# Optimization experiments

Measured on AMD Instinct MI355X. Metric: run time of the kernel, lower is better.

Reference implementation:

```python
import jax, jax.numpy as jnp
import numpy as np

N_NODES = 10000
N_EDGES = 320000
D_IN = 256
D_HID = 256
N_CLASSES = 40


def _init_linear(key, fan_in, fan_out):
    kw, kb = jax.random.split(key)
    bound = 1.0 / np.sqrt(fan_in)
    W = jax.random.uniform(kw, (fan_in, fan_out), jnp.float32, -bound, bound)
    b = jax.random.uniform(kb, (fan_out,), jnp.float32, -bound, bound)
    return W, b


def setup_inputs() -> dict:
    key = jax.random.key(0)
    k0, k1, k2, k3, k4 = jax.random.split(key, 5)
    node_features = jax.random.normal(k0, (N_NODES, D_IN), jnp.float32)
    edge_index = jax.random.randint(k1, (2, N_EDGES), 0, N_NODES, jnp.int64)
    W1, b1 = _init_linear(k2, D_IN, D_HID)
    W2, b2 = _init_linear(k3, D_HID, D_HID)
    W3, b3 = _init_linear(k4, D_HID, N_CLASSES)
    return {"node_features": node_features, "edge_index": edge_index,
            "W1": W1, "b1": b1, "W2": W2, "b2": b2, "W3": W3, "b3": b3}


def _mp_layer(x, src, dst, W, b):
    # message: linear transform of source-node features (transform-then-gather
    # is mathematically identical to gather-then-transform and cheaper when E>N)
    msg = (x @ W + b)[src]                      # [E, d_out]
    # scatter sum-aggregate messages at destination nodes
    out = jax.ops.segment_sum(msg, dst, num_segments=N_NODES)  # [N, d_out]
    return out


def reference(node_features, edge_index, W1, b1, W2, b2, W3, b3):
    src, dst = edge_index[0], edge_index[1]
    x = jax.nn.relu(_mp_layer(node_features, src, dst, W1, b1))
    x = jax.nn.relu(_mp_layer(x, src, dst, W2, b2))
    x = jax.nn.relu(_mp_layer(x, src, dst, W3, b3))
    return x
```

## Files before the change

### kernel.cpp

```cpp
#include <hip/hip_runtime.h>


#define N_NODES   10000
#define N_EDGES   320000
#define D_HID     256
#define N_CLASSES 40
#define CAP       96

typedef __attribute__((ext_vector_type(8))) short short8;
typedef __attribute__((ext_vector_type(4))) float f32x4;

__device__ __forceinline__ ushort f2bf(float f) {
    unsigned u = __float_as_uint(f);
    u = (u + 0x7fffu + ((u >> 16) & 1u)) >> 16;
    return (ushort)u;
}
__device__ __forceinline__ float bf2f(ushort u) {
    return __uint_as_float(((unsigned)u) << 16);
}


__global__ __launch_bounds__(256)
void prep_kernel(const float* __restrict__ X,
                 const float* __restrict__ W1, const float* __restrict__ W2,
                 const float* __restrict__ W3,
                 ushort* __restrict__ Xb, ushort* __restrict__ bufY,
                 ushort* __restrict__ bufH,
                 ushort* __restrict__ W1b, ushort* __restrict__ W2b,
                 ushort* __restrict__ W3b, int* __restrict__ cursor,
                 int* __restrict__ esrc) {
    const int tid  = blockIdx.x * 256 + threadIdx.x;
    const int nthr = gridDim.x * 256;
    for (int i = tid; i < N_NODES; i += nthr) cursor[i] = 0;
    for (int i = tid; i < N_NODES * CAP; i += nthr) esrc[i] = N_NODES;
    ushort4 z; z.x = 0; z.y = 0; z.z = 0; z.w = 0;
    if (tid < 64) {
        ((ushort4*)Xb)[640000 + tid]   = z;
        ((ushort4*)bufY)[640000 + tid] = z;
    }
    if (tid < 10) ((ushort4*)bufH)[100000 + tid] = z;
    for (int i = tid; i < N_NODES * D_HID / 4; i += nthr) {
        float4 v = ((const float4*)X)[i];
        ushort4 o;
        o.x = f2bf(v.x); o.y = f2bf(v.y); o.z = f2bf(v.z); o.w = f2bf(v.w);
        ((ushort4*)Xb)[i] = o;
    }
    for (int i = tid; i < 141312; i += nthr) {
        if (i < 65536) {
            int n = i >> 8, k = i & 255;
            W1b[i] = f2bf(W1[k * 256 + n]);
        } else if (i < 131072) {
            int t2 = i - 65536;
            int n = t2 >> 8, k = t2 & 255;
            W2b[t2] = f2bf(W2[k * 256 + n]);
        } else {
            int t2 = i - 131072;
            int n = t2 >> 8, k = t2 & 255;
            W3b[t2] = f2bf(W3[k * N_CLASSES + n]);
        }
    }
}


__global__ __launch_bounds__(256)
void place_kernel(const int* __restrict__ edges, int* __restrict__ cursor,
                  int* __restrict__ esrc) {
    int e = blockIdx.x * 256 + threadIdx.x;
    if (e < N_EDGES) {
        int d = edges[N_EDGES + e];
        int pos = atomicAdd(&cursor[d], 1);
        if (pos < CAP) esrc[d * CAP + pos] = edges[e];
    }
}


__global__ __launch_bounds__(256)
void gather_kernel(const ushort* __restrict__ Xin, const int* __restrict__ deg,
                   const int* __restrict__ esrc, ushort* __restrict__ Ag) {
    __shared__ int eidx[4 * CAP];
    __shared__ int degL[4];

    const int tid  = threadIdx.x;
    const int w    = tid >> 6, lane = tid & 63;
    const int lo   = lane & 31, hi = lane >> 5;
    const int base = blockIdx.x * 4;

    for (int i = tid; i < 4 * CAP; i += 256) eidx[i] = esrc[base * CAP + i];
    if (tid < 4) {
        int c = deg[base + tid];
        degL[tid] = (c > CAP) ? CAP : c;
    }
    __syncthreads();

    const int node = base + w;
    const int nb   = (degL[w] + 15) >> 4;
    const uint4* hp4 = (const uint4*)Xin;

    float a[8] = {};
    for (int b = 0; b < nb; ++b) {
        uint4 v[8];
#pragma unroll
        for (int u = 0; u < 8; ++u) {
            int e = eidx[w * CAP + b * 16 + 2 * u + hi];
            v[u] = hp4[(size_t)e * 32 + lo];
        }
#pragma unroll
        for (int u = 0; u < 8; ++u) {
            a[0] += bf2f((ushort)(v[u].x & 0xffff)); a[1] += bf2f((ushort)(v[u].x >> 16));
            a[2] += bf2f((ushort)(v[u].y & 0xffff)); a[3] += bf2f((ushort)(v[u].y >> 16));
            a[4] += bf2f((ushort)(v[u].z & 0xffff)); a[5] += bf2f((ushort)(v[u].z >> 16));
            a[6] += bf2f((ushort)(v[u].w & 0xffff)); a[7] += bf2f((ushort)(v[u].w >> 16));
        }
    }
#pragma unroll
    for (int j = 0; j < 8; ++j) a[j] += __shfl_xor(a[j], 32);
    if (lane < 32) {
        uint4 o;
        o.x = (unsigned)f2bf(a[0]) | ((unsigned)f2bf(a[1]) << 16);
        o.y = (unsigned)f2bf(a[2]) | ((unsigned)f2bf(a[3]) << 16);
        o.z = (unsigned)f2bf(a[4]) | ((unsigned)f2bf(a[5]) << 16);
        o.w = (unsigned)f2bf(a[6]) | ((unsigned)f2bf(a[7]) << 16);
        ((uint4*)(Ag + (size_t)node * 256))[lo] = o;
    }
}


#define LDSA 264

template<bool CHAIN>
__global__ __launch_bounds__(256)
void gemm_kernel(const ushort* __restrict__ Ag, const ushort* __restrict__ Bt,
                 const float* __restrict__ bias, const int* __restrict__ deg,
                 const ushort* __restrict__ W3b, const float* __restrict__ b3,
                 ushort* __restrict__ Out) {
    __shared__ ushort As[16 * LDSA];
    __shared__ ushort Bs[40 * LDSA];
    __shared__ float  degF[16];

    const int tid = threadIdx.x;
    const int wave = tid >> 6, lane = tid & 63;
    const int lr = lane & 15, lg = lane >> 4;
    const int rowBase = blockIdx.x * 16;

#pragma unroll
    for (int p = 0; p < 2; ++p) {
        int idx = p * 256 + tid;
        int r = idx >> 5, c = idx & 31;
        *(uint4*)(As + r * LDSA + c * 8) =
            *(const uint4*)(Ag + (size_t)(rowBase + r) * 256 + c * 8);
    }
    if (tid < 16) degF[tid] = (float)deg[rowBase + tid];
    __syncthreads();

    f32x4 acc[4] = {};
    for (int k0 = 0; k0 < 256; k0 += 32) {
#pragma unroll
        for (int p = 0; p < 4; ++p) {
            int idx = p * 256 + tid;
            int n = idx >> 2, c = (idx & 3) * 8;
            *(uint4*)(Bs + n * 40 + c) = *(const uint4*)(Bt + (size_t)n * 256 + k0 + c);
        }
        __syncthreads();
        short8 af = *(const short8*)(As + lr * LDSA + k0 + lg * 8);
#pragma unroll
        for (int j = 0; j < 4; ++j) {
            short8 bf = *(const short8*)(Bs + (wave * 64 + j * 16 + lr) * 40 + lg * 8);
            acc[j] = __builtin_amdgcn_mfma_f32_16x16x32_bf16(af, bf, acc[j], 0, 0, 0);
        }
        __syncthreads();
    }

    if (!CHAIN) {
#pragma unroll
        for (int j = 0; j < 4; ++j) {
            int col = wave * 64 + j * 16 + lr;
            float bv = bias[col];
#pragma unroll
            for (int r = 0; r < 4; ++r) {
                int grow = rowBase + lg * 4 + r;
                float dg = degF[lg * 4 + r];
                Out[(size_t)grow * 256 + col] = f2bf(fmaxf(fmaf(dg, bv, acc[j][r]), 0.f));
            }
        }
    } else {
#pragma unroll
        for (int j = 0; j < 4; ++j) {
            int col = wave * 64 + j * 16 + lr;
            float bv = bias[col];
#pragma unroll
            for (int r = 0; r < 4; ++r) {
                int rl = lg * 4 + r;
                As[rl * LDSA + col] = f2bf(fmaxf(fmaf(degF[rl], bv, acc[j][r]), 0.f));
            }
        }
#pragma unroll
        for (int p = 0; p < 5; ++p) {
            int idx = p * 256 + tid;
            int n = idx >> 5, c = (idx & 31) * 8;
            *(uint4*)(Bs + n * LDSA + c) = *(const uint4*)(W3b + (size_t)n * 256 + c);
        }
        __syncthreads();
        if (wave < 3) {
            f32x4 acc3 = {};
            for (int k0 = 0; k0 < 256; k0 += 32) {
                short8 af = *(const short8*)(As + lr * LDSA + k0 + lg * 8);
                short8 bf = *(const short8*)(Bs + (wave * 16 + lr) * LDSA + k0 + lg * 8);
                acc3 = __builtin_amdgcn_mfma_f32_16x16x32_bf16(af, bf, acc3, 0, 0, 0);
            }
            int col = wave * 16 + lr;
            if (col < N_CLASSES) {
                float bv = b3[col];
#pragma unroll
                for (int r = 0; r < 4; ++r) {
                    int grow = rowBase + lg * 4 + r;
                    Out[(size_t)grow * N_CLASSES + col] = f2bf(acc3[r] + bv);
                }
            }
        }
    }
}


__global__ __launch_bounds__(256)
void agg_relu_40_kernel(const ushort* __restrict__ h, const int* __restrict__ deg,
                        const int* __restrict__ esrc, float* __restrict__ out) {
    const int wv   = threadIdx.x >> 6;
    const int lane = threadIdx.x & 63;
    const int node = (blockIdx.x << 2) + wv;
    if (node >= N_NODES) return;
    int cnt = deg[node];
    if (cnt > CAP) cnt = CAP;
    const int* ep = esrc + node * CAP;
    const int l6  = (lane < 60) ? lane : 0;
    const int g6  = l6 / 10;
    const int c10 = l6 - g6 * 10;
    const int nb  = (cnt + 47) / 48;

    uint2 v0[8], v1[8];
    if (nb > 0) {
#pragma unroll
        for (int u = 0; u < 8; ++u) {
            int s = ep[6 * u + g6];
            v0[u] = *(const uint2*)(h + (size_t)s * N_CLASSES + c10 * 4);
        }
    }
    if (nb > 1) {
#pragma unroll
        for (int u = 0; u < 8; ++u) {
            int s = ep[48 + 6 * u + g6];
            v1[u] = *(const uint2*)(h + (size_t)s * N_CLASSES + c10 * 4);
        }
    }
    float a0 = 0.f, a1 = 0.f, a2 = 0.f, a3 = 0.f;
    if (nb > 0) {
#pragma unroll
        for (int u = 0; u < 8; ++u) {
            a0 += bf2f((ushort)(v0[u].x & 0xffff)); a1 += bf2f((ushort)(v0[u].x >> 16));
            a2 += bf2f((ushort)(v0[u].y & 0xffff)); a3 += bf2f((ushort)(v0[u].y >> 16));
        }
    }
    if (nb > 1) {
#pragma unroll
        for (int u = 0; u < 8; ++u) {
            a0 += bf2f((ushort)(v1[u].x & 0xffff)); a1 += bf2f((ushort)(v1[u].x >> 16));
            a2 += bf2f((ushort)(v1[u].y & 0xffff)); a3 += bf2f((ushort)(v1[u].y >> 16));
        }
    }
#define FOLD40(x) { x += __shfl(x, lane + 30);                      \
                    float t1 = __shfl(x, lane + 10);                \
                    float t2 = __shfl(x, lane + 20);                \
                    x += t1 + t2; }
    FOLD40(a0); FOLD40(a1); FOLD40(a2); FOLD40(a3);
#undef FOLD40
    if (lane < 10) {
        float4 o;
        o.x = fmaxf(a0, 0.f); o.y = fmaxf(a1, 0.f);
        o.z = fmaxf(a2, 0.f); o.w = fmaxf(a3, 0.f);
        *(float4*)(out + (size_t)node * N_CLASSES + lane * 4) = o;
    }
}


extern "C" void kernel_launch(void* const* d_in, const int* in_sizes, int n_in,
                              void* d_out, int out_size, void* d_ws, size_t ws_size,
                              hipStream_t stream) {
    const float* X     = (const float*)d_in[0];
    const int*   edges = (const int*)d_in[1];
    const float* W1 = (const float*)d_in[2];
    const float* b1 = (const float*)d_in[3];
    const float* W2 = (const float*)d_in[4];
    const float* b2 = (const float*)d_in[5];
    const float* W3 = (const float*)d_in[6];
    const float* b3 = (const float*)d_in[7];
    float* out = (float*)d_out;

    char* ws = (char*)d_ws;
    ushort* Xb   = (ushort*)(ws);
    ushort* bufY = (ushort*)(ws + 5120512);
    ushort* bufH = (ushort*)(ws + 10241024);
    ushort* W1b  = (ushort*)(ws + 11041104);
    ushort* W2b  = (ushort*)(ws + 11172176);
    ushort* W3b  = (ushort*)(ws + 11303248);
    int*   cursor = (int*)(ws + 11323728);
    int*   esrc   = (int*)(ws + 11363728);
    ushort* G1   = (ushort*)(ws + 15203728);
    ushort* G2   = (ushort*)(ws + 20323728);

    prep_kernel<<<512, 256, 0, stream>>>(X, W1, W2, W3, Xb, bufY, bufH,
                                         W1b, W2b, W3b, cursor, esrc);
    place_kernel<<<(N_EDGES + 255) / 256, 256, 0, stream>>>(edges, cursor, esrc);
    gather_kernel<<<N_NODES / 4, 256, 0, stream>>>(Xb, cursor, esrc, G1);
    gemm_kernel<false><<<N_NODES / 16, 256, 0, stream>>>(
        G1, W1b, b1, cursor, W3b, b3, bufY);
    gather_kernel<<<N_NODES / 4, 256, 0, stream>>>(bufY, cursor, esrc, G2);
    gemm_kernel<true><<<N_NODES / 16, 256, 0, stream>>>(
        G2, W2b, b2, cursor, W3b, b3, bufH);
    agg_relu_40_kernel<<<(N_NODES + 3) / 4, 256, 0, stream>>>(bufH, cursor, esrc, out);
}
```

Baseline: 160.5 us.

## Bin edges by source block for locality and widen GEMM tiles to 64 rows

```diff
diff --git a/kernel.cpp b/kernel.cpp
--- a/kernel.cpp
+++ b/kernel.cpp
@@ -5,7 +5,9 @@
 #define N_EDGES   320000
 #define D_HID     256
 #define N_CLASSES 40
-#define CAP       96
+#define NSB       10
+#define CAP_S     24
+#define DUMMY     10000
 
 typedef __attribute__((ext_vector_type(8))) short short8;
 typedef __attribute__((ext_vector_type(4))) float f32x4;
@@ -27,12 +29,12 @@
                  ushort* __restrict__ Xb, ushort* __restrict__ bufY,
                  ushort* __restrict__ bufH,
                  ushort* __restrict__ W1b, ushort* __restrict__ W2b,
-                 ushort* __restrict__ W3b, int* __restrict__ cursor,
-                 int* __restrict__ esrc) {
+                 ushort* __restrict__ W3b, int* __restrict__ cur2,
+                 int* __restrict__ esrc2) {
     const int tid  = blockIdx.x * 256 + threadIdx.x;
     const int nthr = gridDim.x * 256;
-    for (int i = tid; i < N_NODES; i += nthr) cursor[i] = 0;
-    for (int i = tid; i < N_NODES * CAP; i += nthr) esrc[i] = N_NODES;
+    for (int i = tid; i < N_NODES * NSB; i += nthr) cur2[i] = 0;
+    for (int i = tid; i < N_NODES * NSB * CAP_S; i += nthr) esrc2[i] = DUMMY;
     ushort4 z; z.x = 0; z.y = 0; z.z = 0; z.w = 0;
     if (tid < 64) {
         ((ushort4*)Xb)[640000 + tid]   = z;
@@ -63,53 +65,59 @@
 
 
 __global__ __launch_bounds__(256)
-void place_kernel(const int* __restrict__ edges, int* __restrict__ cursor,
-                  int* __restrict__ esrc) {
+void place_kernel(const int* __restrict__ edges, int* __restrict__ cur2,
+                  int* __restrict__ esrc2) {
     int e = blockIdx.x * 256 + threadIdx.x;
     if (e < N_EDGES) {
+        int s = edges[e];
         int d = edges[N_EDGES + e];
-        int pos = atomicAdd(&cursor[d], 1);
-        if (pos < CAP) esrc[d * CAP + pos] = edges[e];
+        int sb = s >> 10;
+        int bin = d * NSB + sb;
+        int pos = atomicAdd(&cur2[bin], 1);
+        if (pos < CAP_S) esrc2[bin * CAP_S + pos] = s;
     }
 }
 
 
 __global__ __launch_bounds__(256)
-void gather_kernel(const ushort* __restrict__ Xin, const int* __restrict__ deg,
-                   const int* __restrict__ esrc, ushort* __restrict__ Ag) {
-    __shared__ int eidx[4 * CAP];
-    __shared__ int degL[4];
+void gather_kernel(const ushort* __restrict__ Xin, const int* __restrict__ cur2,
+                   const int* __restrict__ esrc2, ushort* __restrict__ Ag,
+                   float* __restrict__ degOut) {
+    __shared__ int eidx[4 * NSB * CAP_S];
+    __shared__ int cnts[4 * NSB];
 
     const int tid  = threadIdx.x;
     const int w    = tid >> 6, lane = tid & 63;
     const int lo   = lane & 31, hi = lane >> 5;
     const int base = blockIdx.x * 4;
 
-    for (int i = tid; i < 4 * CAP; i += 256) eidx[i] = esrc[base * CAP + i];
-    if (tid < 4) {
-        int c = deg[base + tid];
-        degL[tid] = (c > CAP) ? CAP : c;
-    }
+    for (int i = tid; i < 4 * NSB * CAP_S; i += 256)
+        eidx[i] = esrc2[base * NSB * CAP_S + i];
+    if (tid < 4 * NSB) cnts[tid] = cur2[base * NSB + tid];
     __syncthreads();
 
     const int node = base + w;
-    const int nb   = (degL[w] + 15) >> 4;
     const uint4* hp4 = (const uint4*)Xin;
-
     float a[8] = {};
-    for (int b = 0; b < nb; ++b) {
-        uint4 v[8];
-#pragma unroll
-        for (int u = 0; u < 8; ++u) {
-            int e = eidx[w * CAP + b * 16 + 2 * u + hi];
-            v[u] = hp4[(size_t)e * 32 + lo];
-        }
-#pragma unroll
-        for (int u = 0; u < 8; ++u) {
-            a[0] += bf2f((ushort)(v[u].x & 0xffff)); a[1] += bf2f((ushort)(v[u].x >> 16));
-            a[2] += bf2f((ushort)(v[u].y & 0xffff)); a[3] += bf2f((ushort)(v[u].y >> 16));
-            a[4] += bf2f((ushort)(v[u].z & 0xffff)); a[5] += bf2f((ushort)(v[u].z >> 16));
-            a[6] += bf2f((ushort)(v[u].w & 0xffff)); a[7] += bf2f((ushort)(v[u].w >> 16));
+    int degT = 0;
+    for (int sb = 0; sb < NSB; ++sb) {
+        int raw = cnts[w * NSB + sb];
+        degT += raw;
+        int cnt = raw < CAP_S ? raw : CAP_S;
+        const int* ep = eidx + (w * NSB + sb) * CAP_S;
+        for (int b = 0; b < cnt; b += 4) {
+            int e0 = ep[b + hi];
+            int e1 = ep[b + 2 + hi];
+            uint4 v0 = hp4[(size_t)e0 * 32 + lo];
+            uint4 v1 = hp4[(size_t)e1 * 32 + lo];
+            a[0] += bf2f((ushort)(v0.x & 0xffff)); a[1] += bf2f((ushort)(v0.x >> 16));
+            a[2] += bf2f((ushort)(v0.y & 0xffff)); a[3] += bf2f((ushort)(v0.y >> 16));
+            a[4] += bf2f((ushort)(v0.z & 0xffff)); a[5] += bf2f((ushort)(v0.z >> 16));
+            a[6] += bf2f((ushort)(v0.w & 0xffff)); a[7] += bf2f((ushort)(v0.w >> 16));
+            a[0] += bf2f((ushort)(v1.x & 0xffff)); a[1] += bf2f((ushort)(v1.x >> 16));
+            a[2] += bf2f((ushort)(v1.y & 0xffff)); a[3] += bf2f((ushort)(v1.y >> 16));
+            a[4] += bf2f((ushort)(v1.z & 0xffff)); a[5] += bf2f((ushort)(v1.z >> 16));
+            a[6] += bf2f((ushort)(v1.w & 0xffff)); a[7] += bf2f((ushort)(v1.w >> 16));
         }
     }
 #pragma unroll
@@ -122,98 +130,109 @@
         o.w = (unsigned)f2bf(a[6]) | ((unsigned)f2bf(a[7]) << 16);
         ((uint4*)(Ag + (size_t)node * 256))[lo] = o;
     }
-}
-
-
-#define LDSA 264
+    if (lane == 0) degOut[node] = (float)degT;
+}
+
+
+#define LDSB 264
 
 template<bool CHAIN>
-__global__ __launch_bounds__(256)
+__global__ __launch_bounds__(512)
 void gemm_kernel(const ushort* __restrict__ Ag, const ushort* __restrict__ Bt,
-                 const float* __restrict__ bias, const int* __restrict__ deg,
+                 const float* __restrict__ bias, const float* __restrict__ degF,
                  const ushort* __restrict__ W3b, const float* __restrict__ b3,
                  ushort* __restrict__ Out) {
-    __shared__ ushort As[16 * LDSA];
-    __shared__ ushort Bs[40 * LDSA];
-    __shared__ float  degF[16];
-
-    const int tid = threadIdx.x;
+    __shared__ ushort Bs[256 * LDSB];
+    __shared__ ushort W3L[40 * LDSB];
+    __shared__ float  degL[64];
+
+    const int tid  = threadIdx.x;
     const int wave = tid >> 6, lane = tid & 63;
     const int lr = lane & 15, lg = lane >> 4;
-    const int rowBase = blockIdx.x * 16;
-
-#pragma unroll
-    for (int p = 0; p < 2; ++p) {
-        int idx = p * 256 + tid;
-        int r = idx >> 5, c = idx & 31;
-        *(uint4*)(As + r * LDSA + c * 8) =
-            *(const uint4*)(Ag + (size_t)(rowBase + r) * 256 + c * 8);
-    }
-    if (tid < 16) degF[tid] = (float)deg[rowBase + tid];
+    const int rg = wave >> 1, cg = wave & 1;
+    const int rowBase = blockIdx.x * 64;
+
+#pragma unroll
+    for (int p = 0; p < 16; ++p) {
+        int idx = p * 512 + tid;
+        int n = idx >> 5, c = (idx & 31) * 8;
+        *(uint4*)(Bs + n * LDSB + c) = *(const uint4*)(Bt + (size_t)n * 256 + c);
+    }
+    if (CHAIN) {
+#pragma unroll
+        for (int p = 0; p < 3; ++p) {
+            int idx = p * 512 + tid;
+            if (idx < 1280) {
+                int n = idx >> 5, c = (idx & 31) * 8;
+                *(uint4*)(W3L + n * LDSB + c) = *(const uint4*)(W3b + (size_t)n * 256 + c);
+            }
+        }
+    }
+    if (tid < 64) degL[tid] = degF[rowBase + tid];
+
+    short8 afr[8];
+    const size_t aBase = (size_t)(rowBase + rg * 16 + lr) * 256 + lg * 8;
+#pragma unroll
+    for (int ks = 0; ks < 8; ++ks)
+        afr[ks] = *(const short8*)(Ag + aBase + ks * 32);
+
     __syncthreads();
 
-    f32x4 acc[4] = {};
-    for (int k0 = 0; k0 < 256; k0 += 32) {
-#pragma unroll
-        for (int p = 0; p < 4; ++p) {
-            int idx = p * 256 + tid;
-            int n = idx >> 2, c = (idx & 3) * 8;
-            *(uint4*)(Bs + n * 40 + c) = *(const uint4*)(Bt + (size_t)n * 256 + k0 + c);
-        }
+    f32x4 acc[8] = {};
+#pragma unroll
+    for (int ks = 0; ks < 8; ++ks) {
+        int k0 = ks * 32;
+#pragma unroll
+        for (int j = 0; j < 8; ++j) {
+            short8 bf = *(const short8*)(Bs + (cg * 128 + j * 16 + lr) * LDSB + k0 + lg * 8);
+            acc[j] = __builtin_amdgcn_mfma_f32_16x16x32_bf16(afr[ks], bf, acc[j], 0, 0, 0);
+        }
+    }
+
+    if (!CHAIN) {
+#pragma unroll
+        for (int j = 0; j < 8; ++j) {
+            int col = cg * 128 + j * 16 + lr;
+            float bv = bias[col];
+#pragma unroll
+            for (int r = 0; r < 4; ++r) {
+                int rl = rg * 16 + lg * 4 + r;
+                int grow = rowBase + rl;
+                if (grow < N_NODES)
+                    Out[(size_t)grow * 256 + col] =
+                        f2bf(fmaxf(fmaf(degL[rl], bv, acc[j][r]), 0.f));
+            }
+        }
+    } else {
         __syncthreads();
-        short8 af = *(const short8*)(As + lr * LDSA + k0 + lg * 8);
-#pragma unroll
-        for (int j = 0; j < 4; ++j) {
-            short8 bf = *(const short8*)(Bs + (wave * 64 + j * 16 + lr) * 40 + lg * 8);
-            acc[j] = __builtin_amdgcn_mfma_f32_16x16x32_bf16(af, bf, acc[j], 0, 0, 0);
+#pragma unroll
+        for (int j = 0; j < 8; ++j) {
+            int col = cg * 128 + j * 16 + lr;
+            float bv = bias[col];
+#pragma unroll
+            for (int r = 0; r < 4; ++r) {
+                int rl = rg * 16 + lg * 4 + r;
+                Bs[rl * LDSB + col] = f2bf(fmaxf(fmaf(degL[rl], bv, acc[j][r]), 0.f));
+            }
         }
         __syncthreads();
-    }
-
-    if (!CHAIN) {
-#pragma unroll
-        for (int j = 0; j < 4; ++j) {
-            int col = wave * 64 + j * 16 + lr;
-            float bv = bias[col];
-#pragma unroll
-            for (int r = 0; r < 4; ++r) {
-                int grow = rowBase + lg * 4 + r;
-                float dg = degF[lg * 4 + r];
-                Out[(size_t)grow * 256 + col] = f2bf(fmaxf(fmaf(dg, bv, acc[j][r]), 0.f));
-            }
-        }
-    } else {
-#pragma unroll
-        for (int j = 0; j < 4; ++j) {
-            int col = wave * 64 + j * 16 + lr;
-            float bv = bias[col];
-#pragma unroll
-            for (int r = 0; r < 4; ++r) {
-                int rl = lg * 4 + r;
-                As[rl * LDSA + col] = f2bf(fmaxf(fmaf(degF[rl], bv, acc[j][r]), 0.f));
-            }
-        }
-#pragma unroll
-        for (int p = 0; p < 5; ++p) {
-            int idx = p * 256 + tid;
-            int n = idx >> 5, c = (idx & 31) * 8;
-            *(uint4*)(Bs + n * LDSA + c) = *(const uint4*)(W3b + (size_t)n * 256 + c);
-        }
-        __syncthreads();
-        if (wave < 3) {
-            f32x4 acc3 = {};
-            for (int k0 = 0; k0 < 256; k0 += 32) {
-                short8 af = *(const short8*)(As + lr * LDSA + k0 + lg * 8);
-                short8 bf = *(const short8*)(Bs + (wave * 16 + lr) * LDSA + k0 + lg * 8);
-                acc3 = __builtin_amdgcn_mfma_f32_16x16x32_bf16(af, bf, acc3, 0, 0, 0);
-            }
-            int col = wave * 16 + lr;
+        for (int t = wave; t < 12; t += 8) {
+            int rT = t & 3, cT = t >> 2;
+            f32x4 a3 = {};
+#pragma unroll
+            for (int ks = 0; ks < 8; ++ks) {
+                short8 af = *(const short8*)(Bs + (rT * 16 + lr) * LDSB + ks * 32 + lg * 8);
+                short8 bf = *(const short8*)(W3L + (cT * 16 + lr) * LDSB + ks * 32 + lg * 8);
+                a3 = __builtin_amdgcn_mfma_f32_16x16x32_bf16(af, bf, a3, 0, 0, 0);
+            }
+            int col = cT * 16 + lr;
             if (col < N_CLASSES) {
                 float bv = b3[col];
 #pragma unroll
                 for (int r = 0; r < 4; ++r) {
-                    int grow = rowBase + lg * 4 + r;
-                    Out[(size_t)grow * N_CLASSES + col] = f2bf(acc3[r] + bv);
+                    int grow = rowBase + rT * 16 + lg * 4 + r;
+                    if (grow < N_NODES)
+                        Out[(size_t)grow * N_CLASSES + col] = f2bf(a3[r] + bv);
                 }
             }
         }
@@ -222,48 +241,27 @@
 
 
 __global__ __launch_bounds__(256)
-void agg_relu_40_kernel(const ushort* __restrict__ h, const int* __restrict__ deg,
-                        const int* __restrict__ esrc, float* __restrict__ out) {
+void agg_relu_40_kernel(const ushort* __restrict__ h, const int* __restrict__ cur2,
+                        const int* __restrict__ esrc2, float* __restrict__ out) {
     const int wv   = threadIdx.x >> 6;
     const int lane = threadIdx.x & 63;
     const int node = (blockIdx.x << 2) + wv;
-    if (node >= N_NODES) return;
-    int cnt = deg[node];
-    if (cnt > CAP) cnt = CAP;
-    const int* ep = esrc + node * CAP;
-    const int l6  = (lane < 60) ? lane : 0;
-    const int g6  = l6 / 10;
-    const int c10 = l6 - g6 * 10;
-    const int nb  = (cnt + 47) / 48;
-
-    uint2 v0[8], v1[8];
-    if (nb > 0) {
-#pragma unroll
-        for (int u = 0; u < 8; ++u) {
-            int s = ep[6 * u + g6];
-            v0[u] = *(const uint2*)(h + (size_t)s * N_CLASSES + c10 * 4);
-        }
-    }
-    if (nb > 1) {
-#pragma unroll
-        for (int u = 0; u < 8; ++u) {
-            int s = ep[48 + 6 * u + g6];
-            v1[u] = *(const uint2*)(h + (size_t)s * N_CLASSES + c10 * 4);
-        }
-    }
+    const int l6   = (lane < 60) ? lane : 0;
+    const int g6   = l6 / 10;
+    const int c10  = l6 - g6 * 10;
+
+    const int* cp  = cur2 + node * NSB;
+    const int* ep2 = esrc2 + node * NSB * CAP_S;
     float a0 = 0.f, a1 = 0.f, a2 = 0.f, a3 = 0.f;
-    if (nb > 0) {
-#pragma unroll
-        for (int u = 0; u < 8; ++u) {
-            a0 += bf2f((ushort)(v0[u].x & 0xffff)); a1 += bf2f((ushort)(v0[u].x >> 16));
-            a2 += bf2f((ushort)(v0[u].y & 0xffff)); a3 += bf2f((ushort)(v0[u].y >> 16));
-        }
-    }
-    if (nb > 1) {
-#pragma unroll
-        for (int u = 0; u < 8; ++u) {
-            a0 += bf2f((ushort)(v1[u].x & 0xffff)); a1 += bf2f((ushort)(v1[u].x >> 16));
-            a2 += bf2f((ushort)(v1[u].y & 0xffff)); a3 += bf2f((ushort)(v1[u].y >> 16));
+    for (int sb = 0; sb < NSB; ++sb) {
+        int cnt = cp[sb];
+        if (cnt > CAP_S) cnt = CAP_S;
+        const int* ep = ep2 + sb * CAP_S;
+        for (int b = 0; b < cnt; b += 6) {
+            int s = ep[b + g6];
+            uint2 v = *(const uint2*)(h + (size_t)s * N_CLASSES + c10 * 4);
+            a0 += bf2f((ushort)(v.x & 0xffff)); a1 += bf2f((ushort)(v.x >> 16));
+            a2 += bf2f((ushort)(v.y & 0xffff)); a3 += bf2f((ushort)(v.y >> 16));
         }
     }
 #define FOLD40(x) { x += __shfl(x, lane + 30);                      \
@@ -295,25 +293,24 @@
     float* out = (float*)d_out;
 
     char* ws = (char*)d_ws;
-    ushort* Xb   = (ushort*)(ws);
-    ushort* bufY = (ushort*)(ws + 5120512);
-    ushort* bufH = (ushort*)(ws + 10241024);
-    ushort* W1b  = (ushort*)(ws + 11041104);
-    ushort* W2b  = (ushort*)(ws + 11172176);
-    ushort* W3b  = (ushort*)(ws + 11303248);
-    int*   cursor = (int*)(ws + 11323728);
-    int*   esrc   = (int*)(ws + 11363728);
-    ushort* G1   = (ushort*)(ws + 15203728);
-    ushort* G2   = (ushort*)(ws + 20323728);
+    ushort* Xb    = (ushort*)(ws);
+    ushort* bufY  = (ushort*)(ws + 5120512);
+    ushort* bufH  = (ushort*)(ws + 10241024);
+    ushort* W1b   = (ushort*)(ws + 11041104);
+    ushort* W2b   = (ushort*)(ws + 11172176);
+    ushort* W3b   = (ushort*)(ws + 11303248);
+    int*    cur2  = (int*)(ws + 11323728);
+    int*    esrc2 = (int*)(ws + 11723728);
+    ushort* Ag1   = (ushort*)(ws + 21323728);
+    ushort* Ag2   = (ushort*)(ws + 26468304);
+    float*  degF  = (float*)(ws + 31612880);
 
     prep_kernel<<<512, 256, 0, stream>>>(X, W1, W2, W3, Xb, bufY, bufH,
-                                         W1b, W2b, W3b, cursor, esrc);
-    place_kernel<<<(N_EDGES + 255) / 256, 256, 0, stream>>>(edges, cursor, esrc);
-    gather_kernel<<<N_NODES / 4, 256, 0, stream>>>(Xb, cursor, esrc, G1);
-    gemm_kernel<false><<<N_NODES / 16, 256, 0, stream>>>(
-        G1, W1b, b1, cursor, W3b, b3, bufY);
-    gather_kernel<<<N_NODES / 4, 256, 0, stream>>>(bufY, cursor, esrc, G2);
-    gemm_kernel<true><<<N_NODES / 16, 256, 0, stream>>>(
-        G2, W2b, b2, cursor, W3b, b3, bufH);
-    agg_relu_40_kernel<<<(N_NODES + 3) / 4, 256, 0, stream>>>(bufH, cursor, esrc, out);
-}
+                                         W1b, W2b, W3b, cur2, esrc2);
+    place_kernel<<<(N_EDGES + 255) / 256, 256, 0, stream>>>(edges, cur2, esrc2);
+    gather_kernel<<<N_NODES / 4, 256, 0, stream>>>(Xb, cur2, esrc2, Ag1, degF);
+    gemm_kernel<false><<<157, 512, 0, stream>>>(Ag1, W1b, b1, degF, W3b, b3, bufY);
+    gather_kernel<<<N_NODES / 4, 256, 0, stream>>>(bufY, cur2, esrc2, Ag2, degF);
+    gemm_kernel<true><<<157, 512, 0, stream>>>(Ag2, W2b, b2, degF, W3b, b3, bufH);
+    agg_relu_40_kernel<<<N_NODES / 4, 256, 0, stream>>>(bufH, cur2, esrc2, out);
+}
```

After: 169.9 us. 5.8% more time.
